# Kernel tuning notes

Measured on AMD Instinct MI355X. Metric: run time of the kernel, lower is better.

The kernel has to match this reference:

```python
import jax, jax.numpy as jnp
import numpy as np

SEQ_LEN = 256
BATCH = 128
TAGS = 48
START_TAG = 46
END_TAG = 47
NINF = -100000.0


def setup_inputs() -> dict:
    key = jax.random.key(0)
    k1, k2, k3 = jax.random.split(key, 3)
    scores = jax.random.normal(k1, (BATCH, SEQ_LEN, TAGS, TAGS), dtype=jnp.float32)
    # target: True = tag forbidden at this position (partial-annotation constraint mask)
    target = jax.random.bernoulli(k2, 0.3, (BATCH, SEQ_LEN, TAGS))
    # mask: valid (non-pad) positions, contiguous prefixes of random length
    lengths = jax.random.randint(k3, (BATCH,), SEQ_LEN // 2, SEQ_LEN + 1)
    mask = jnp.arange(SEQ_LEN)[None, :] < lengths[:, None]
    return {"scores": scores, "target": target, "mask": mask}


def _lse_dim1(v):
    # v: (B, T_from, T_to) -> logsumexp over T_from -> (B, T_to)
    m = jnp.max(v, axis=1, keepdims=True)
    return (m + jnp.log(jnp.sum(jnp.exp(v - m), axis=1, keepdims=True)))[:, 0, :]


def reference(scores, target, mask):
    # transpose to time-major, matching the torch module's .transpose(1, 0)
    scores_t = jnp.transpose(scores, (1, 0, 2, 3))  # (S, B, T, T)
    target_t = jnp.transpose(target, (1, 0, 2))     # (S, B, T)
    mask_t = jnp.transpose(mask, (1, 0))            # (S, B)

    init_vals = scores_t[0, :, START_TAG, :]        # (B, T)
    partition0 = init_vals
    tag_partition0 = jnp.where(target_t[0], NINF, init_vals)

    def step(carry, xs):
        partition, tag_partition = carry
        cur, tgt, m = xs  # (B,T,T), (B,T), (B,)
        cur_tag_partition = jnp.where(tgt, NINF, _lse_dim1(cur + tag_partition[:, :, None]))
        cur_partition = _lse_dim1(cur + partition[:, :, None])
        mm = m[:, None]
        partition = jnp.where(mm, cur_partition, partition)
        tag_partition = jnp.where(mm, cur_tag_partition, tag_partition)
        return (partition, tag_partition), None

    (partition, tag_partition), _ = jax.lax.scan(
        step, (partition0, tag_partition0),
        (scores_t[1:], target_t[1:], mask_t[1:]))

    tp = tag_partition[:, END_TAG]
    tp = jnp.where(tp == NINF, 0.0, tp)
    loss = jnp.sum(partition[:, END_TAG]) - jnp.sum(tp)
    return loss
```

## Files before the change

### kernel.cpp

```cpp
#include <hip/hip_runtime.h>


constexpr int SEQ = 256;
constexpr int NTAG = 48;
constexpr int START_TAG = 46;
constexpr int END_TAG = 47;
constexpr float L2E = 1.4426950408889634f;
constexpr float LN2 = 0.6931471805599453f;
constexpr int W = 4;
constexpr int C = 12;

constexpr int SLAB = NTAG * NTAG * 4;
constexpr int NBUF = 6;
constexpr int BUFS = NBUF * SLAB;
constexpr int PART_OFF = BUFS + 192;
constexpr int TGT_OFF  = PART_OFF + 2048;
constexpr int LDS_TOT  = TGT_OFF + 12352;

__device__ __forceinline__ float fexp2(float x) { return __builtin_amdgcn_exp2f(x); }
__device__ __forceinline__ float flog2(float x) { return __builtin_amdgcn_logf(x); }
__device__ __forceinline__ float rlane(float v, int l) {
    return __uint_as_float(__builtin_amdgcn_readlane(__float_as_uint(v), l));
}

__global__ __launch_bounds__(256, 1)
void crf_chain_kernel(const float* __restrict__ S,
                      const void* __restrict__ tgtv,
                      const void* __restrict__ mskv,
                      float* __restrict__ ws)
{
    __shared__ __align__(16) unsigned char lds[LDS_TOT];
    const int bid  = blockIdx.x;
    const int b    = bid & 127;
    const int tagc = bid >> 7;
    const int tid  = threadIdx.x;
    const int k    = tid >> 6;
    const int j    = tid & 63;
    const bool jok = (j < NTAG);
    const int jj   = jok ? j : 0;
    const int i0   = k * C;

    const bool pack8 = (((const int*)mskv)[0] != 1);
    const unsigned char* msk8  = (const unsigned char*)mskv;
    const int*           msk32 = (const int*)mskv;

    int len = 0;
    #pragma unroll
    for (int r = 0; r < 4; ++r) {
        int idx = b * SEQ + r * 64 + j;
        int mm = pack8 ? (msk8[idx] != 0) : (msk32[idx] != 0);
        len += (int)__popcll(__ballot(mm));
    }

    if (tagc) {
        if (pack8) {
            const int4* src = (const int4*)((const unsigned char*)tgtv + (size_t)b * 12288);
            int4* dst = (int4*)(lds + TGT_OFF);
            #pragma unroll
            for (int r = 0; r < 3; ++r) dst[tid * 3 + r] = src[tid * 3 + r];
        } else {
            const int4* src = (const int4*)((const int*)tgtv + (size_t)b * 12288);
            unsigned* dst = (unsigned*)(lds + TGT_OFF);
            #pragma unroll
            for (int r = 0; r < 12; ++r) {
                int4 v = src[tid * 12 + r];
                dst[tid * 12 + r] = (unsigned)((v.x & 1) | ((v.y & 1) << 8) |
                                               ((v.z & 1) << 16) | ((v.w & 1) << 24));
            }
        }
    }
    if (tid < 12) *(float4*)(lds + BUFS + tid * 16) = make_float4(0.f, 0.f, 0.f, 0.f);
    if (tid < 4)  *(float4*)(lds + TGT_OFF + 12288 + tid * 16) = make_float4(0.f, 0.f, 0.f, 0.f);
    __syncthreads();

    const size_t sbf = (size_t)b * SEQ * NTAG * NTAG;
    const float  bias = jok ? 0.0f : -200.0f;

    float st0 = S[sbf + START_TAG * NTAG + jj] * L2E;
    if (!jok) st0 = -1e30f;
    float M0 = st0;
    #pragma unroll
    for (int off = 1; off < 64; off <<= 1) M0 = fmaxf(M0, __shfl_xor(M0, off));
    float u = jok ? fexp2(st0 - M0) : 0.0f;
    if (tagc && jok) {
        int tv0 = lds[TGT_OFF + j];
        if (tv0) u = 0.0f;
    }
    float Mg = M0;

    const unsigned char* Sb = (const unsigned char*)S + sbf * 4;
    const int lo16 = k * 2304 + j * 16;
    const int lo4  = k * 2304 + 2048 + j * 4;

    auto stage = [&](int tau, int slot) {
        const unsigned char* g = Sb + (size_t)tau * SLAB;
        unsigned char* l = lds + slot * SLAB + k * 2304;
        __builtin_amdgcn_global_load_lds(
            (const __attribute__((address_space(1))) void*)(g + lo16),
            (__attribute__((address_space(3))) void*)l, 16, 0, 0);
        __builtin_amdgcn_global_load_lds(
            (const __attribute__((address_space(1))) void*)(g + lo16 + 1024),
            (__attribute__((address_space(3))) void*)(l + 1024), 16, 0, 0);
        __builtin_amdgcn_global_load_lds(
            (const __attribute__((address_space(1))) void*)(g + lo4),
            (__attribute__((address_space(3))) void*)(l + 2048), 4, 0, 0);
    };

    #pragma unroll
    for (int tau = 1; tau <= 5; ++tau) stage(tau, tau);
    asm volatile("s_waitcnt vmcnt(9)" ::: "memory");
    __builtin_amdgcn_sched_barrier(0);

    float EA[C], EB[C];
    {
        const float* ep = (const float*)(lds + 1 * SLAB + i0 * 192);
        #pragma unroll
        for (int c = 0; c < C; ++c) EA[c] = fexp2(fmaf(ep[c * 48 + j], L2E, bias));
    }

    float* part = (float*)(lds + PART_OFF);
    const unsigned char* tl = lds + TGT_OFF;
    int st_slot = 0;
    int rd_slot = 2;

    auto body = [&](float (&Ecur)[C], float (&Enext)[C], int t, int pb) {
        int tvv = 0;
        if (tagc) tvv = tl[t * 48 + j];
        float p0 = 0.f, p1 = 0.f;
        #pragma unroll
        for (int c = 0; c < C; c += 2) {
            p0 = fmaf(Ecur[c],     rlane(u, i0 + c),     p0);
            p1 = fmaf(Ecur[c + 1], rlane(u, i0 + c + 1), p1);
        }
        part[pb * 256 + k * 64 + j] = p0 + p1;
        int tau = (t + 5 < len) ? (t + 5) : (len - 1);
        stage(tau, st_slot);
        if (++st_slot >= NBUF) st_slot = 0;
        if (t + 1 < len) {
            const float* ep = (const float*)(lds + rd_slot * SLAB + i0 * 192);
            #pragma unroll
            for (int c = 0; c < C; ++c)
                Enext[c] = fexp2(fmaf(ep[c * 48 + j], L2E, bias));
        }
        if (++rd_slot >= NBUF) rd_slot = 0;
        __builtin_amdgcn_sched_barrier(0);
        asm volatile("s_waitcnt lgkmcnt(0)" ::: "memory");
        asm volatile("s_waitcnt vmcnt(9)" ::: "memory");
        __builtin_amdgcn_sched_barrier(0);
        __builtin_amdgcn_s_barrier();
        __builtin_amdgcn_sched_barrier(0);
        float q0 = part[pb * 256 + j]       + part[pb * 256 + 64 + j];
        float q1 = part[pb * 256 + 128 + j] + part[pb * 256 + 192 + j];
        float un = q0 + q1;
        if (tagc && tvv) un = 0.0f;
        if (!jok) un = 0.0f;
        if ((t & 7) == 0) {
            float mx = un;
            #pragma unroll
            for (int off = 1; off < 64; off <<= 1) mx = fmaxf(mx, __shfl_xor(mx, off));
            int ex = (int)((__float_as_uint(mx) >> 23) & 0xFF) - 126;
            un = ldexpf(un, -ex);
            Mg += (float)ex;
        }
        u = un;
    };

    int t = 1;
    for (; t + 1 < len; t += 2) {
        body(EA, EB, t, 1);
        body(EB, EA, t + 1, 0);
    }
    if (t < len) body(EA, EB, t, 1);

    if (k == 0 && j == END_TAG) {
        float r = (Mg + flog2(u)) * LN2;
        if (tagc) r = (u == 0.0f) ? 0.0f : -r;
        ws[bid] = r;
    }
}

__global__ void crf_reduce_kernel(const float* __restrict__ ws, float* __restrict__ out)
{
    int l = threadIdx.x;
    float v = (ws[l] + ws[l + 64]) + (ws[l + 128] + ws[l + 192]);
    #pragma unroll
    for (int off = 32; off > 0; off >>= 1) v += __shfl_down(v, off);
    if (l == 0) out[0] = v;
}

extern "C" void kernel_launch(void* const* d_in, const int* in_sizes, int n_in,
                              void* d_out, int out_size, void* d_ws, size_t ws_size,
                              hipStream_t stream)
{
    const float* S   = (const float*)d_in[0];
    const void*  tgt = d_in[1];
    const void*  msk = d_in[2];
    float* out = (float*)d_out;
    float* ws  = (float*)d_ws;

    crf_chain_kernel<<<256, 256, 0, stream>>>(S, tgt, msk, ws);
    crf_reduce_kernel<<<1, 64, 0, stream>>>(ws, out);
}
```

Baseline: 130.2 us.

## Split recurrence over eight waves per block with six rows each

```diff
diff --git a/kernel.cpp b/kernel.cpp
--- a/kernel.cpp
+++ b/kernel.cpp
@@ -7,14 +7,15 @@
 constexpr int END_TAG = 47;
 constexpr float L2E = 1.4426950408889634f;
 constexpr float LN2 = 0.6931471805599453f;
-constexpr int W = 4;
-constexpr int C = 12;
+constexpr int W = 8;
+constexpr int C = 6;
 
 constexpr int SLAB = NTAG * NTAG * 4;
+constexpr int SLOT = SLAB + 128;
 constexpr int NBUF = 6;
-constexpr int BUFS = NBUF * SLAB;
-constexpr int PART_OFF = BUFS + 192;
-constexpr int TGT_OFF  = PART_OFF + 2048;
+constexpr int RING = NBUF * SLOT;
+constexpr int PART_OFF = RING;
+constexpr int TGT_OFF  = PART_OFF + 4096;
 constexpr int LDS_TOT  = TGT_OFF + 12352;
 
 __device__ __forceinline__ float fexp2(float x) { return __builtin_amdgcn_exp2f(x); }
@@ -23,7 +24,7 @@
     return __uint_as_float(__builtin_amdgcn_readlane(__float_as_uint(v), l));
 }
 
-__global__ __launch_bounds__(256, 1)
+__global__ __launch_bounds__(512, 1)
 void crf_chain_kernel(const float* __restrict__ S,
                       const void* __restrict__ tgtv,
                       const void* __restrict__ mskv,
@@ -57,20 +58,22 @@
             const int4* src = (const int4*)((const unsigned char*)tgtv + (size_t)b * 12288);
             int4* dst = (int4*)(lds + TGT_OFF);
             #pragma unroll
-            for (int r = 0; r < 3; ++r) dst[tid * 3 + r] = src[tid * 3 + r];
+            for (int r = 0; r < 2; ++r) {
+                int w = r * 512 + tid;
+                if (w < 768) dst[w] = src[w];
+            }
         } else {
             const int4* src = (const int4*)((const int*)tgtv + (size_t)b * 12288);
             unsigned* dst = (unsigned*)(lds + TGT_OFF);
             #pragma unroll
-            for (int r = 0; r < 12; ++r) {
-                int4 v = src[tid * 12 + r];
-                dst[tid * 12 + r] = (unsigned)((v.x & 1) | ((v.y & 1) << 8) |
-                                               ((v.z & 1) << 16) | ((v.w & 1) << 24));
+            for (int r = 0; r < 6; ++r) {
+                int w = r * 512 + tid;
+                int4 v = src[w];
+                dst[w] = (unsigned)((v.x & 1) | ((v.y & 1) << 8) |
+                                    ((v.z & 1) << 16) | ((v.w & 1) << 24));
             }
         }
     }
-    if (tid < 12) *(float4*)(lds + BUFS + tid * 16) = make_float4(0.f, 0.f, 0.f, 0.f);
-    if (tid < 4)  *(float4*)(lds + TGT_OFF + 12288 + tid * 16) = make_float4(0.f, 0.f, 0.f, 0.f);
     __syncthreads();
 
     const size_t sbf = (size_t)b * SEQ * NTAG * NTAG;
@@ -89,31 +92,29 @@
     float Mg = M0;
 
     const unsigned char* Sb = (const unsigned char*)S + sbf * 4;
-    const int lo16 = k * 2304 + j * 16;
-    const int lo4  = k * 2304 + 2048 + j * 4;
+    const int lo16 = k * 1152 + j * 16;
+    const int lo4  = k * 1152 + 1024 + j * 4;
 
     auto stage = [&](int tau, int slot) {
         const unsigned char* g = Sb + (size_t)tau * SLAB;
-        unsigned char* l = lds + slot * SLAB + k * 2304;
+        unsigned char* l = lds + slot * SLOT + k * 1152;
         __builtin_amdgcn_global_load_lds(
             (const __attribute__((address_space(1))) void*)(g + lo16),
             (__attribute__((address_space(3))) void*)l, 16, 0, 0);
-        __builtin_amdgcn_global_load_lds(
-            (const __attribute__((address_space(1))) void*)(g + lo16 + 1024),
-            (__attribute__((address_space(3))) void*)(l + 1024), 16, 0, 0);
-        __builtin_amdgcn_global_load_lds(
-            (const __attribute__((address_space(1))) void*)(g + lo4),
-            (__attribute__((address_space(3))) void*)(l + 2048), 4, 0, 0);
+        if (j < 32)
+            __builtin_amdgcn_global_load_lds(
+                (const __attribute__((address_space(1))) void*)(g + lo4),
+                (__attribute__((address_space(3))) void*)(l + 1024), 4, 0, 0);
     };
 
     #pragma unroll
     for (int tau = 1; tau <= 5; ++tau) stage(tau, tau);
-    asm volatile("s_waitcnt vmcnt(9)" ::: "memory");
+    asm volatile("s_waitcnt vmcnt(6)" ::: "memory");
     __builtin_amdgcn_sched_barrier(0);
 
     float EA[C], EB[C];
     {
-        const float* ep = (const float*)(lds + 1 * SLAB + i0 * 192);
+        const float* ep = (const float*)(lds + 1 * SLOT + i0 * 192);
         #pragma unroll
         for (int c = 0; c < C; ++c) EA[c] = fexp2(fmaf(ep[c * 48 + j], L2E, bias));
     }
@@ -132,12 +133,12 @@
             p0 = fmaf(Ecur[c],     rlane(u, i0 + c),     p0);
             p1 = fmaf(Ecur[c + 1], rlane(u, i0 + c + 1), p1);
         }
-        part[pb * 256 + k * 64 + j] = p0 + p1;
+        part[pb * 512 + k * 64 + j] = p0 + p1;
         int tau = (t + 5 < len) ? (t + 5) : (len - 1);
         stage(tau, st_slot);
         if (++st_slot >= NBUF) st_slot = 0;
         if (t + 1 < len) {
-            const float* ep = (const float*)(lds + rd_slot * SLAB + i0 * 192);
+            const float* ep = (const float*)(lds + rd_slot * SLOT + i0 * 192);
             #pragma unroll
             for (int c = 0; c < C; ++c)
                 Enext[c] = fexp2(fmaf(ep[c * 48 + j], L2E, bias));
@@ -145,13 +146,16 @@
         if (++rd_slot >= NBUF) rd_slot = 0;
         __builtin_amdgcn_sched_barrier(0);
         asm volatile("s_waitcnt lgkmcnt(0)" ::: "memory");
-        asm volatile("s_waitcnt vmcnt(9)" ::: "memory");
+        asm volatile("s_waitcnt vmcnt(6)" ::: "memory");
         __builtin_amdgcn_sched_barrier(0);
         __builtin_amdgcn_s_barrier();
         __builtin_amdgcn_sched_barrier(0);
-        float q0 = part[pb * 256 + j]       + part[pb * 256 + 64 + j];
-        float q1 = part[pb * 256 + 128 + j] + part[pb * 256 + 192 + j];
-        float un = q0 + q1;
+        const float* pp = part + pb * 512 + j;
+        float q0 = pp[0]   + pp[64];
+        float q1 = pp[128] + pp[192];
+        float q2 = pp[256] + pp[320];
+        float q3 = pp[384] + pp[448];
+        float un = (q0 + q1) + (q2 + q3);
         if (tagc && tvv) un = 0.0f;
         if (!jok) un = 0.0f;
         if ((t & 7) == 0) {
@@ -198,6 +202,6 @@
     float* out = (float*)d_out;
     float* ws  = (float*)d_ws;
 
-    crf_chain_kernel<<<256, 256, 0, stream>>>(S, tgt, msk, ws);
+    crf_chain_kernel<<<256, 512, 0, stream>>>(S, tgt, msk, ws);
     crf_reduce_kernel<<<1, 64, 0, stream>>>(ws, out);
 }
```

Result: slower. 144.1 us (+10.7%).

## Parallelize CRF forward recursion over time segments with MFMA matrix products

Applied to the files above, without the earlier changes.

```diff
diff --git a/kernel.cpp b/kernel.cpp
--- a/kernel.cpp
+++ b/kernel.cpp
@@ -7,29 +7,221 @@
 constexpr int END_TAG = 47;
 constexpr float L2E = 1.4426950408889634f;
 constexpr float LN2 = 0.6931471805599453f;
-constexpr int W = 4;
-constexpr int C = 12;
-
-constexpr int SLAB = NTAG * NTAG * 4;
-constexpr int NBUF = 6;
-constexpr int BUFS = NBUF * SLAB;
-constexpr int PART_OFF = BUFS + 192;
-constexpr int TGT_OFF  = PART_OFF + 2048;
-constexpr int LDS_TOT  = TGT_OFF + 12352;
-
-__device__ __forceinline__ float fexp2(float x) { return __builtin_amdgcn_exp2f(x); }
-__device__ __forceinline__ float flog2(float x) { return __builtin_amdgcn_logf(x); }
-__device__ __forceinline__ float rlane(float v, int l) {
+constexpr int NSEG = 16;
+constexpr int SEGL = 16;
+
+constexpr size_t QFLOATS = (size_t)128 * 2 * NSEG * 2304;
+constexpr size_t QBYTES  = QFLOATS * 4;
+constexpr size_t EXBYTES = (size_t)128 * 2 * NSEG * 4;
+constexpr size_t RBYTES  = 256 * 4;
+constexpr size_t WS_NEED = QBYTES + EXBYTES + RBYTES;
+
+typedef float    f32x4 __attribute__((ext_vector_type(4)));
+typedef _Float16 f16x4 __attribute__((ext_vector_type(4)));
+
+__device__ __forceinline__ float fexp2(float x){ return __builtin_amdgcn_exp2f(x); }
+__device__ __forceinline__ float flog2(float x){ return __builtin_amdgcn_logf(x); }
+__device__ __forceinline__ float rlane(float v, int l){
     return __uint_as_float(__builtin_amdgcn_readlane(__float_as_uint(v), l));
 }
 
+__global__ __launch_bounds__(256, 2)
+void crf_seg_kernel(const float* __restrict__ S, const void* __restrict__ tgtv,
+                    const void* __restrict__ mskv, float* __restrict__ wsQ,
+                    int* __restrict__ wsE)
+{
+    const int g     = blockIdx.x * 4 + (threadIdx.x >> 6);
+    const int b     = g >> 5;
+    const int seg   = (g >> 1) & 15;
+    const int chain = g & 1;
+    const int l = threadIdx.x & 63, m = l & 15, q = l >> 4;
+
+    const bool pack8 = (((const int*)mskv)[0] != 1);
+    const unsigned char* msk8  = (const unsigned char*)mskv;
+    const int*           msk32 = (const int*)mskv;
+    const unsigned char* tgt8  = (const unsigned char*)tgtv;
+    const int*           tgt32 = (const int*)tgtv;
+
+    int len = 0;
+    #pragma unroll
+    for (int r = 0; r < 4; ++r) {
+        int idx = b * SEQ + r * 64 + l;
+        int mm = pack8 ? (msk8[idx] != 0) : (msk32[idx] != 0);
+        len += (int)__popcll(__ballot(mm));
+    }
+
+    const int a = 1 + seg * SEGL;
+    const int tend = min(a + SEGL, len);
+
+    f32x4 acc[3][3];
+    #pragma unroll
+    for (int R = 0; R < 3; ++R)
+        #pragma unroll
+        for (int Cc = 0; Cc < 3; ++Cc)
+            #pragma unroll
+            for (int r = 0; r < 4; ++r)
+                acc[R][Cc][r] = (R == Cc && (q * 4 + r) == m) ? 1.0f : 0.0f;
+
+    float sc = 1.0f;
+    int   E  = 0;
+
+    for (int t = a; t < tend; ++t) {
+        const float* Sb = S + ((size_t)(b * SEQ + t)) * 2304;
+        bool tm[3] = {false, false, false};
+        if (chain) {
+            int tb = (b * SEQ + t) * NTAG + m;
+            if (pack8) { tm[0] = tgt8[tb] != 0;  tm[1] = tgt8[tb + 16] != 0;  tm[2] = tgt8[tb + 32] != 0; }
+            else       { tm[0] = tgt32[tb] != 0; tm[1] = tgt32[tb + 16] != 0; tm[2] = tgt32[tb + 32] != 0; }
+        }
+        f16x4 bfr[3][3];
+        #pragma unroll
+        for (int kb = 0; kb < 3; ++kb)
+            #pragma unroll
+            for (int Cc = 0; Cc < 3; ++Cc)
+                #pragma unroll
+                for (int e = 0; e < 4; ++e)
+                    bfr[kb][Cc][e] = (_Float16)(acc[kb][Cc][e] * sc);
+        f16x4 afr[3][3];
+        #pragma unroll
+        for (int M0 = 0; M0 < 3; ++M0) {
+            const bool kill = chain && tm[M0];
+            #pragma unroll
+            for (int kb = 0; kb < 3; ++kb)
+                #pragma unroll
+                for (int e = 0; e < 4; ++e) {
+                    float v = Sb[(kb * 16 + q * 4 + e) * 48 + M0 * 16 + m];
+                    afr[M0][kb][e] = kill ? (_Float16)0.0f
+                                          : (_Float16)fexp2(v * L2E);
+                }
+        }
+        float mx = 0.0f;
+        #pragma unroll
+        for (int M0 = 0; M0 < 3; ++M0)
+            #pragma unroll
+            for (int Cc = 0; Cc < 3; ++Cc) {
+                f32x4 d = {0.0f, 0.0f, 0.0f, 0.0f};
+                d = __builtin_amdgcn_mfma_f32_16x16x16f16(afr[M0][0], bfr[0][Cc], d, 0, 0, 0);
+                d = __builtin_amdgcn_mfma_f32_16x16x16f16(afr[M0][1], bfr[1][Cc], d, 0, 0, 0);
+                d = __builtin_amdgcn_mfma_f32_16x16x16f16(afr[M0][2], bfr[2][Cc], d, 0, 0, 0);
+                acc[M0][Cc] = d;
+                mx = fmaxf(mx, fmaxf(fmaxf(d[0], d[1]), fmaxf(d[2], d[3])));
+            }
+        #pragma unroll
+        for (int off = 1; off < 64; off <<= 1) mx = fmaxf(mx, __shfl_xor(mx, off));
+        int ex = (int)((__float_as_uint(mx) >> 23) & 0xFF) - 126;
+        sc = __uint_as_float((unsigned)(127 - ex) << 23);
+        E += ex;
+    }
+
+    float* Qo = wsQ + ((size_t)((b * 2 + chain) * NSEG + seg)) * 2304;
+    #pragma unroll
+    for (int R = 0; R < 3; ++R)
+        #pragma unroll
+        for (int Cc = 0; Cc < 3; ++Cc)
+            #pragma unroll
+            for (int r = 0; r < 4; ++r)
+                Qo[(16 * R + q * 4 + r) * 48 + 16 * Cc + m] = acc[R][Cc][r] * sc;
+    if (l == 0) wsE[(b * 2 + chain) * NSEG + seg] = E;
+}
+
+__global__ __launch_bounds__(64)
+void crf_comb_kernel(const float* __restrict__ S, const void* __restrict__ tgtv,
+                     const void* __restrict__ mskv, const float* __restrict__ wsQ,
+                     const int* __restrict__ wsE, float* __restrict__ wsR)
+{
+    const int bid = blockIdx.x;
+    const int b = bid >> 1, chain = bid & 1;
+    const int l = threadIdx.x;
+    const bool jok = (l < NTAG);
+    const int j = jok ? l : 0;
+
+    const bool pack8 = (((const int*)mskv)[0] != 1);
+    const unsigned char* tgt8  = (const unsigned char*)tgtv;
+    const int*           tgt32 = (const int*)tgtv;
+
+    float st0 = S[(size_t)b * SEQ * 2304 + START_TAG * 48 + j] * L2E;
+    if (!jok) st0 = -1e30f;
+    float M0 = st0;
+    #pragma unroll
+    for (int off = 1; off < 64; off <<= 1) M0 = fmaxf(M0, __shfl_xor(M0, off));
+    float u = jok ? fexp2(st0 - M0) : 0.0f;
+    if (chain && jok) {
+        int ti = b * SEQ * NTAG + j;
+        int tv0 = pack8 ? (int)tgt8[ti] : tgt32[ti];
+        if (tv0) u = 0.0f;
+    }
+    float eu = M0;
+
+    const int eb = (b * 2 + chain) * NSEG;
+    const float* Qb = wsQ + (size_t)eb * 2304 + (size_t)(jok ? l : 47) * 48;
+
+    float4 qa[12], qb[12];
+    #pragma unroll
+    for (int i = 0; i < 12; ++i) qa[i] = *(const float4*)(Qb + i * 4);
+
+    auto step = [&](float4 (&qx)[12], int s) {
+        float a0 = 0.f, a1 = 0.f, a2 = 0.f, a3 = 0.f;
+        #pragma unroll
+        for (int i = 0; i < 12; ++i) {
+            a0 = fmaf(qx[i].x, rlane(u, 4 * i + 0), a0);
+            a1 = fmaf(qx[i].y, rlane(u, 4 * i + 1), a1);
+            a2 = fmaf(qx[i].z, rlane(u, 4 * i + 2), a2);
+            a3 = fmaf(qx[i].w, rlane(u, 4 * i + 3), a3);
+        }
+        float un = (a0 + a1) + (a2 + a3);
+        if (!jok) un = 0.0f;
+        float mx = un;
+        #pragma unroll
+        for (int off = 1; off < 64; off <<= 1) mx = fmaxf(mx, __shfl_xor(mx, off));
+        int ex = (int)((__float_as_uint(mx) >> 23) & 0xFF) - 126;
+        un *= __uint_as_float((unsigned)(127 - ex) << 23);
+        eu += (float)(ex + wsE[eb + s]);
+        u = un;
+    };
+
+    #pragma unroll
+    for (int p = 0; p < 8; ++p) {
+        #pragma unroll
+        for (int i = 0; i < 12; ++i)
+            qb[i] = *(const float4*)(Qb + (size_t)(2 * p + 1) * 2304 + i * 4);
+        step(qa, 2 * p);
+        if (p < 7) {
+            #pragma unroll
+            for (int i = 0; i < 12; ++i)
+                qa[i] = *(const float4*)(Qb + (size_t)(2 * p + 2) * 2304 + i * 4);
+        }
+        step(qb, 2 * p + 1);
+    }
+
+    if (l == END_TAG) {
+        float r = (flog2(u) + eu) * LN2;
+        if (chain) r = (u == 0.0f) ? 0.0f : -r;
+        wsR[bid] = r;
+    }
+}
+
+__global__ void crf_reduce_kernel(const float* __restrict__ ws, float* __restrict__ out)
+{
+    int l = threadIdx.x;
+    float v = (ws[l] + ws[l + 64]) + (ws[l + 128] + ws[l + 192]);
+    #pragma unroll
+    for (int off = 32; off > 0; off >>= 1) v += __shfl_down(v, off);
+    if (l == 0) out[0] = v;
+}
+
+constexpr int FB_C = 12;
+constexpr int FB_SLAB = NTAG * NTAG * 4;
+constexpr int FB_NBUF = 6;
+constexpr int FB_BUFS = FB_NBUF * FB_SLAB;
+constexpr int FB_PART_OFF = FB_BUFS + 192;
+constexpr int FB_TGT_OFF  = FB_PART_OFF + 2048;
+constexpr int FB_LDS_TOT  = FB_TGT_OFF + 12352;
+
 __global__ __launch_bounds__(256, 1)
-void crf_chain_kernel(const float* __restrict__ S,
-                      const void* __restrict__ tgtv,
-                      const void* __restrict__ mskv,
-                      float* __restrict__ ws)
-{
-    __shared__ __align__(16) unsigned char lds[LDS_TOT];
+void fb_chain_kernel(const float* __restrict__ S, const void* __restrict__ tgtv,
+                     const void* __restrict__ mskv, float* __restrict__ ws)
+{
+    __shared__ __align__(16) unsigned char lds[FB_LDS_TOT];
     const int bid  = blockIdx.x;
     const int b    = bid & 127;
     const int tagc = bid >> 7;
@@ -38,7 +230,7 @@
     const int j    = tid & 63;
     const bool jok = (j < NTAG);
     const int jj   = jok ? j : 0;
-    const int i0   = k * C;
+    const int i0   = k * FB_C;
 
     const bool pack8 = (((const int*)mskv)[0] != 1);
     const unsigned char* msk8  = (const unsigned char*)mskv;
@@ -55,12 +247,12 @@
     if (tagc) {
         if (pack8) {
             const int4* src = (const int4*)((const unsigned char*)tgtv + (size_t)b * 12288);
-            int4* dst = (int4*)(lds + TGT_OFF);
+            int4* dst = (int4*)(lds + FB_TGT_OFF);
             #pragma unroll
             for (int r = 0; r < 3; ++r) dst[tid * 3 + r] = src[tid * 3 + r];
         } else {
             const int4* src = (const int4*)((const int*)tgtv + (size_t)b * 12288);
-            unsigned* dst = (unsigned*)(lds + TGT_OFF);
+            unsigned* dst = (unsigned*)(lds + FB_TGT_OFF);
             #pragma unroll
             for (int r = 0; r < 12; ++r) {
                 int4 v = src[tid * 12 + r];
@@ -69,8 +261,8 @@
             }
         }
     }
-    if (tid < 12) *(float4*)(lds + BUFS + tid * 16) = make_float4(0.f, 0.f, 0.f, 0.f);
-    if (tid < 4)  *(float4*)(lds + TGT_OFF + 12288 + tid * 16) = make_float4(0.f, 0.f, 0.f, 0.f);
+    if (tid < 12) *(float4*)(lds + FB_BUFS + tid * 16) = make_float4(0.f, 0.f, 0.f, 0.f);
+    if (tid < 4)  *(float4*)(lds + FB_TGT_OFF + 12288 + tid * 16) = make_float4(0.f, 0.f, 0.f, 0.f);
     __syncthreads();
 
     const size_t sbf = (size_t)b * SEQ * NTAG * NTAG;
@@ -83,7 +275,7 @@
     for (int off = 1; off < 64; off <<= 1) M0 = fmaxf(M0, __shfl_xor(M0, off));
     float u = jok ? fexp2(st0 - M0) : 0.0f;
     if (tagc && jok) {
-        int tv0 = lds[TGT_OFF + j];
+        int tv0 = lds[FB_TGT_OFF + j];
         if (tv0) u = 0.0f;
     }
     float Mg = M0;
@@ -93,59 +285,59 @@
     const int lo4  = k * 2304 + 2048 + j * 4;
 
     auto stage = [&](int tau, int slot) {
-        const unsigned char* g = Sb + (size_t)tau * SLAB;
-        unsigned char* l = lds + slot * SLAB + k * 2304;
+        const unsigned char* gp = Sb + (size_t)tau * FB_SLAB;
+        unsigned char* lp = lds + slot * FB_SLAB + k * 2304;
         __builtin_amdgcn_global_load_lds(
-            (const __attribute__((address_space(1))) void*)(g + lo16),
-            (__attribute__((address_space(3))) void*)l, 16, 0, 0);
+            (const __attribute__((address_space(1))) void*)(gp + lo16),
+            (__attribute__((address_space(3))) void*)lp, 16, 0, 0);
         __builtin_amdgcn_global_load_lds(
-            (const __attribute__((address_space(1))) void*)(g + lo16 + 1024),
-            (__attribute__((address_space(3))) void*)(l + 1024), 16, 0, 0);
+            (const __attribute__((address_space(1))) void*)(gp + lo16 + 1024),
+            (__attribute__((address_space(3))) void*)(lp + 1024), 16, 0, 0);
         __builtin_amdgcn_global_load_lds(
-            (const __attribute__((address_space(1))) void*)(g + lo4),
-            (__attribute__((address_space(3))) void*)(l + 2048), 4, 0, 0);
+            (const __attribute__((address_space(1))) void*)(gp + lo4),
+            (__attribute__((address_space(3))) void*)(lp + 2048), 4, 0, 0);
     };
 
     #pragma unroll
     for (int tau = 1; tau <= 5; ++tau) stage(tau, tau);
-    asm volatile("s_waitcnt vmcnt(9)" ::: "memory");
+    asm volatile("s_waitcnt vmcnt(6)" ::: "memory");
     __builtin_amdgcn_sched_barrier(0);
 
-    float EA[C], EB[C];
+    float EA[FB_C], EB[FB_C];
     {
-        const float* ep = (const float*)(lds + 1 * SLAB + i0 * 192);
-        #pragma unroll
-        for (int c = 0; c < C; ++c) EA[c] = fexp2(fmaf(ep[c * 48 + j], L2E, bias));
-    }
-
-    float* part = (float*)(lds + PART_OFF);
-    const unsigned char* tl = lds + TGT_OFF;
+        const float* ep = (const float*)(lds + 1 * FB_SLAB + i0 * 192);
+        #pragma unroll
+        for (int c = 0; c < FB_C; ++c) EA[c] = fexp2(fmaf(ep[c * 48 + j], L2E, bias));
+    }
+
+    float* part = (float*)(lds + FB_PART_OFF);
+    const unsigned char* tl = lds + FB_TGT_OFF;
     int st_slot = 0;
     int rd_slot = 2;
 
-    auto body = [&](float (&Ecur)[C], float (&Enext)[C], int t, int pb) {
+    auto body = [&](float (&Ecur)[FB_C], float (&Enext)[FB_C], int t, int pb) {
         int tvv = 0;
         if (tagc) tvv = tl[t * 48 + j];
         float p0 = 0.f, p1 = 0.f;
         #pragma unroll
-        for (int c = 0; c < C; c += 2) {
+        for (int c = 0; c < FB_C; c += 2) {
             p0 = fmaf(Ecur[c],     rlane(u, i0 + c),     p0);
             p1 = fmaf(Ecur[c + 1], rlane(u, i0 + c + 1), p1);
         }
         part[pb * 256 + k * 64 + j] = p0 + p1;
         int tau = (t + 5 < len) ? (t + 5) : (len - 1);
         stage(tau, st_slot);
-        if (++st_slot >= NBUF) st_slot = 0;
+        if (++st_slot >= FB_NBUF) st_slot = 0;
         if (t + 1 < len) {
-            const float* ep = (const float*)(lds + rd_slot * SLAB + i0 * 192);
-            #pragma unroll
-            for (int c = 0; c < C; ++c)
+            const float* ep = (const float*)(lds + rd_slot * FB_SLAB + i0 * 192);
+            #pragma unroll
+            for (int c = 0; c < FB_C; ++c)
                 Enext[c] = fexp2(fmaf(ep[c * 48 + j], L2E, bias));
         }
-        if (++rd_slot >= NBUF) rd_slot = 0;
+        if (++rd_slot >= FB_NBUF) rd_slot = 0;
         __builtin_amdgcn_sched_barrier(0);
         asm volatile("s_waitcnt lgkmcnt(0)" ::: "memory");
-        asm volatile("s_waitcnt vmcnt(9)" ::: "memory");
+        asm volatile("s_waitcnt vmcnt(6)" ::: "memory");
         __builtin_amdgcn_sched_barrier(0);
         __builtin_amdgcn_s_barrier();
         __builtin_amdgcn_sched_barrier(0);
@@ -179,15 +371,6 @@
     }
 }
 
-__global__ void crf_reduce_kernel(const float* __restrict__ ws, float* __restrict__ out)
-{
-    int l = threadIdx.x;
-    float v = (ws[l] + ws[l + 64]) + (ws[l + 128] + ws[l + 192]);
-    #pragma unroll
-    for (int off = 32; off > 0; off >>= 1) v += __shfl_down(v, off);
-    if (l == 0) out[0] = v;
-}
-
 extern "C" void kernel_launch(void* const* d_in, const int* in_sizes, int n_in,
                               void* d_out, int out_size, void* d_ws, size_t ws_size,
                               hipStream_t stream)
@@ -196,8 +379,17 @@
     const void*  tgt = d_in[1];
     const void*  msk = d_in[2];
     float* out = (float*)d_out;
-    float* ws  = (float*)d_ws;
-
-    crf_chain_kernel<<<256, 256, 0, stream>>>(S, tgt, msk, ws);
-    crf_reduce_kernel<<<1, 64, 0, stream>>>(ws, out);
-}
+
+    if (ws_size >= WS_NEED) {
+        float* wsQ = (float*)d_ws;
+        int*   wsE = (int*)((char*)d_ws + QBYTES);
+        float* wsR = (float*)((char*)d_ws + QBYTES + EXBYTES);
+        crf_seg_kernel<<<1024, 256, 0, stream>>>(S, tgt, msk, wsQ, wsE);
+        crf_comb_kernel<<<256, 64, 0, stream>>>(S, tgt, msk, wsQ, wsE, wsR);
+        crf_reduce_kernel<<<1, 64, 0, stream>>>(wsR, out);
+    } else {
+        float* ws = (float*)d_ws;
+        fb_chain_kernel<<<256, 256, 0, stream>>>(S, tgt, msk, ws);
+        crf_reduce_kernel<<<1, 64, 0, stream>>>(ws, out);
+    }
+}
```

After: 287.7 us. 2.21x slower.
